# Optimization experiments

Measured on AMD Instinct MI355X. Metric: run time of the kernel, lower is better.

Reference implementation:

```python
import jax, jax.numpy as jnp
import numpy as np

D_IN, D_MODEL = 512, 256
B, N = 2, 512


def setup_inputs() -> dict:
    key = jax.random.key(0)
    ks = jax.random.split(key, 8)
    xav_x = float(np.sqrt(2.0 / (D_IN + D_MODEL)))
    xav_p = float(np.sqrt(2.0 / (4 + D_MODEL)))
    return {
        "x": jax.random.normal(ks[0], (B, N, D_IN), dtype=jnp.float32),
        "pos": jax.random.normal(ks[1], (B, N, 4), dtype=jnp.float32),
        "attn_mask": jax.random.randint(ks[2], (B, N, N), 0, 2, dtype=jnp.int32),
        "Wx": jax.random.normal(ks[3], (D_IN, D_MODEL), dtype=jnp.float32) * xav_x,
        "bx": jnp.zeros((D_MODEL,), dtype=jnp.float32),
        "Wp": jax.random.normal(ks[4], (4, D_MODEL), dtype=jnp.float32) * xav_p,
        "bp": jnp.zeros((D_MODEL,), dtype=jnp.float32),
        "w": jax.random.normal(ks[5], (D_MODEL,), dtype=jnp.float32) * 0.05,
    }


def reference(x, pos, attn_mask, Wx, bx, Wp, bp, w):
    # projected, activated inputs: [B, N, d_model]
    h = jnp.tanh(x @ Wx + bx)
    # pairwise relative positions: [B, N, N, 4]
    rel = pos[:, :, None, :] - pos[:, None, :, :]
    # position MLP + tanh: [B, N, N, d_model]
    z = jnp.tanh(rel @ Wp + bp)
    # scores via dot with weight vector: [B, N, N]
    attn = jnp.einsum("bijd,d->bij", z, w)
    mask = attn_mask != 0
    attn = jnp.where(mask, attn, -jnp.inf)
    attn = jax.nn.softmax(attn, axis=2)
    attn = jnp.where(mask, attn, 0.0)
    # dropout is identity in eval mode
    # weighted sum: [B, N, d_model]
    output = jnp.einsum("bij,bjd->bid", attn, h)
    return (output, attn)
```

## Files before the change

### kernel.cpp

```cpp
#include <hip/hip_runtime.h>
#include <hip/hip_bf16.h>
#include <math.h>

#define BATCH   2
#define SEQ     512
#define DIN     512
#define DM      256

#define LOG2E2  2.88539008177792681f

#if __has_builtin(__builtin_amdgcn_exp2f)
#define EXP2(x) __builtin_amdgcn_exp2f(x)
#else
#define EXP2(x) exp2f(x)
#endif
#if __has_builtin(__builtin_amdgcn_rcpf)
#define RCP(x) __builtin_amdgcn_rcpf(x)
#else
#define RCP(x) (1.0f / (x))
#endif

__device__ __forceinline__ float tanh_from_scaled(float targ) {
    return fmaf(-2.0f, RCP(1.0f + EXP2(targ)), 1.0f);
}

__global__ __launch_bounds__(512) void produce_k(
    const float* __restrict__ pos,
    const float* __restrict__ Wp,
    const float* __restrict__ x,
    const float* __restrict__ Wx,
    const float* __restrict__ bx,
    float* __restrict__ EBf,
    float* __restrict__ h)
{
    const int tid = threadIdx.x;

    if (blockIdx.x < 128) {
        const int b  = blockIdx.x >> 6;
        const int q  = blockIdx.x & 63;
        const int d0 = 4 * q;
        const float4 p = ((const float4*)pos)[b * SEQ + tid];
        #pragma unroll
        for (int i = 0; i < 4; i++) {
            const int d = d0 + i;
            const float P = fmaf(p.x, Wp[d], fmaf(p.y, Wp[DM + d],
                            fmaf(p.z, Wp[2*DM + d], p.w * Wp[3*DM + d])));
            EBf[((size_t)(b * DM + d)) * SEQ + tid] = EXP2(-LOG2E2 * P);
        }
        return;
    }

    __shared__ float  s_xt[2][32][68];
    __shared__ float  s_wt[2][64][32];
    __shared__ float4 s_part[256];

    const int idx = blockIdx.x - 128;
    const int rt  = idx >> 3;
    const int ct  = idx & 7;
    const int kh  = __builtin_amdgcn_readfirstlane(tid >> 8);
    const int t   = tid & 255;
    const int ty  = t >> 3;
    const int tx  = t & 7;
    const int row = rt * 32 + ty;

    float4 acc = make_float4(0.f, 0.f, 0.f, 0.f);

    for (int ks = 0; ks < 4; ks++) {
        const int k0 = kh * 256 + ks * 64;
        #pragma unroll
        for (int s = 0; s < 2; s++) {
            const int fidx = t * 2 + s;
            const int r = fidx >> 4, c = fidx & 15;
            *(float4*)&s_xt[kh][r][4 * c] =
                *(const float4*)(x + (size_t)(rt * 32 + r) * DIN + k0 + 4 * c);
        }
        #pragma unroll
        for (int s = 0; s < 2; s++) {
            const int fidx = t * 2 + s;
            const int r = fidx >> 3, c = fidx & 7;
            *(float4*)&s_wt[kh][r][4 * c] =
                *(const float4*)(Wx + (size_t)(k0 + r) * DM + ct * 32 + 4 * c);
        }
        __syncthreads();

        #pragma unroll 8
        for (int k = 0; k < 64; k++) {
            const float  xv = s_xt[kh][ty][k];
            const float4 wq = *(const float4*)&s_wt[kh][k][4 * tx];
            acc.x = fmaf(xv, wq.x, acc.x);
            acc.y = fmaf(xv, wq.y, acc.y);
            acc.z = fmaf(xv, wq.z, acc.z);
            acc.w = fmaf(xv, wq.w, acc.w);
        }
        __syncthreads();
    }

    if (kh == 1) s_part[t] = acc;
    __syncthreads();
    if (kh == 0) {
        const float4 q4 = s_part[t];
        const float4 bq = *(const float4*)(bx + ct * 32 + 4 * tx);
        float4 o;
        o.x = tanh_from_scaled(LOG2E2 * (acc.x + q4.x + bq.x));
        o.y = tanh_from_scaled(LOG2E2 * (acc.y + q4.y + bq.y));
        o.z = tanh_from_scaled(LOG2E2 * (acc.z + q4.z + bq.z));
        o.w = tanh_from_scaled(LOG2E2 * (acc.w + q4.w + bq.w));
        *(float4*)(h + (size_t)row * DM + ct * 32 + 4 * tx) = o;
    }
}

__global__ __launch_bounds__(512) void attend_k(
    const float* __restrict__ pos,
    const float* __restrict__ Wp,
    const float* __restrict__ bp,
    const int*   __restrict__ mask,
    const float* __restrict__ wv,
    const float* __restrict__ EBf,
    const float* __restrict__ h,
    float* __restrict__ out,
    float* __restrict__ attn_out)
{
    const int b   = blockIdx.x >> 7;
    const int i0  = (blockIdx.x & 127) * 4;
    const int tid = threadIdx.x;
    const int l   = tid & 63;

    __shared__ float4 s_ea[DM];
    __shared__ float  s_p[4][SEQ];
    __shared__ float  s_red[4][8];
    __shared__ float  s_o[7][4][DM];

    {
        const int d  = tid & 255;
        const int rp = __builtin_amdgcn_readfirstlane(tid >> 8);
        const int r0 = rp * 2;
        const float4 p0 = ((const float4*)pos)[b * SEQ + i0 + r0];
        const float4 p1 = ((const float4*)pos)[b * SEQ + i0 + r0 + 1];
        const float wp0 = Wp[d], wp1 = Wp[DM + d], wp2 = Wp[2*DM + d], wp3 = Wp[3*DM + d];
        const float bpd = bp[d];
        const float P0 = fmaf(p0.x, wp0, fmaf(p0.y, wp1, fmaf(p0.z, wp2, p0.w * wp3)));
        const float P1 = fmaf(p1.x, wp0, fmaf(p1.y, wp1, fmaf(p1.z, wp2, p1.w * wp3)));
        float* se = (float*)&s_ea[d];
        se[r0]     = EXP2(LOG2E2 * (P0 + bpd));
        se[r0 + 1] = EXP2(LOG2E2 * (P1 + bpd));
    }
    __syncthreads();

    const float* __restrict__ EBj = EBf + (size_t)b * DM * SEQ + tid;

    float a0 = 0.f, a1 = 0.f, a2 = 0.f, a3 = 0.f;
    #pragma unroll 8
    for (int t = 0; t < 128; t++) {
        const float eb0 = EBj[(size_t)(2*t) * SEQ];
        const float eb1 = EBj[(size_t)(2*t + 1) * SEQ];
        const float4 eA = s_ea[2*t];
        const float4 eB = s_ea[2*t + 1];
        const float w0 = wv[2*t];
        const float w1 = wv[2*t + 1];

        {
            const float y0 = fmaf(eA.x, eb0, 1.f), y1 = fmaf(eB.x, eb1, 1.f);
            a0 = fmaf(fmaf(w0, y1, w1 * y0), RCP(y0 * y1), a0);
        }
        {
            const float y0 = fmaf(eA.y, eb0, 1.f), y1 = fmaf(eB.y, eb1, 1.f);
            a1 = fmaf(fmaf(w0, y1, w1 * y0), RCP(y0 * y1), a1);
        }
        {
            const float y0 = fmaf(eA.z, eb0, 1.f), y1 = fmaf(eB.z, eb1, 1.f);
            a2 = fmaf(fmaf(w0, y1, w1 * y0), RCP(y0 * y1), a2);
        }
        {
            const float y0 = fmaf(eA.w, eb0, 1.f), y1 = fmaf(eB.w, eb1, 1.f);
            a3 = fmaf(fmaf(w0, y1, w1 * y0), RCP(y0 * y1), a3);
        }
    }

    const size_t mrow = (size_t)b * SEQ * SEQ + (size_t)i0 * SEQ + tid;
    const int m0 = mask[mrow];
    const int m1 = mask[mrow + SEQ];
    const int m2 = mask[mrow + 2*SEQ];
    const int m3 = mask[mrow + 3*SEQ];
    float p0 = m0 ? EXP2(-LOG2E2 * a0) : 0.f;
    float p1 = m1 ? EXP2(-LOG2E2 * a1) : 0.f;
    float p2 = m2 ? EXP2(-LOG2E2 * a2) : 0.f;
    float p3 = m3 ? EXP2(-LOG2E2 * a3) : 0.f;

    float s0 = p0, s1 = p1, s2 = p2, s3 = p3;
    #pragma unroll
    for (int off = 32; off; off >>= 1) {
        s0 += __shfl_xor(s0, off, 64);
        s1 += __shfl_xor(s1, off, 64);
        s2 += __shfl_xor(s2, off, 64);
        s3 += __shfl_xor(s3, off, 64);
    }
    const int w = tid >> 6;
    if (l == 0) { s_red[0][w] = s0; s_red[1][w] = s1; s_red[2][w] = s2; s_red[3][w] = s3; }
    __syncthreads();

    {
        const float4 r0a = ((const float4*)s_red[0])[0], r0b = ((const float4*)s_red[0])[1];
        const float4 r1a = ((const float4*)s_red[1])[0], r1b = ((const float4*)s_red[1])[1];
        const float4 r2a = ((const float4*)s_red[2])[0], r2b = ((const float4*)s_red[2])[1];
        const float4 r3a = ((const float4*)s_red[3])[0], r3b = ((const float4*)s_red[3])[1];
        p0 *= __fdividef(1.0f, (r0a.x+r0a.y+r0a.z+r0a.w) + (r0b.x+r0b.y+r0b.z+r0b.w));
        p1 *= __fdividef(1.0f, (r1a.x+r1a.y+r1a.z+r1a.w) + (r1b.x+r1b.y+r1b.z+r1b.w));
        p2 *= __fdividef(1.0f, (r2a.x+r2a.y+r2a.z+r2a.w) + (r2b.x+r2b.y+r2b.z+r2b.w));
        p3 *= __fdividef(1.0f, (r3a.x+r3a.y+r3a.z+r3a.w) + (r3b.x+r3b.y+r3b.z+r3b.w));
    }

    attn_out[mrow]         = p0;
    attn_out[mrow + SEQ]   = p1;
    attn_out[mrow + 2*SEQ] = p2;
    attn_out[mrow + 3*SEQ] = p3;
    s_p[0][tid] = p0; s_p[1][tid] = p1; s_p[2][tid] = p2; s_p[3][tid] = p3;
    __syncthreads();

    const int dq = tid & 63;
    const int js = __builtin_amdgcn_readfirstlane(tid >> 6);
    const float* __restrict__ hp = h + (size_t)(b * SEQ + js * 64) * DM + 4 * dq;
    const float* __restrict__ q0p = &s_p[0][js * 64];
    const float* __restrict__ q1p = &s_p[1][js * 64];
    const float* __restrict__ q2p = &s_p[2][js * 64];
    const float* __restrict__ q3p = &s_p[3][js * 64];

    float4 a0v = make_float4(0,0,0,0), a1v = a0v, a2v = a0v, a3v = a0v;
    #pragma unroll 4
    for (int jj = 0; jj < 16; jj++) {
        const float4 P0 = *(const float4*)(q0p + 4 * jj);
        const float4 P1 = *(const float4*)(q1p + 4 * jj);
        const float4 P2 = *(const float4*)(q2p + 4 * jj);
        const float4 P3 = *(const float4*)(q3p + 4 * jj);
        const float4 h0 = *(const float4*)(hp + (size_t)(4*jj + 0) * DM);
        const float4 h1 = *(const float4*)(hp + (size_t)(4*jj + 1) * DM);
        const float4 h2 = *(const float4*)(hp + (size_t)(4*jj + 2) * DM);
        const float4 h3 = *(const float4*)(hp + (size_t)(4*jj + 3) * DM);

        a0v.x = fmaf(P0.x,h0.x,fmaf(P0.y,h1.x,fmaf(P0.z,h2.x,fmaf(P0.w,h3.x,a0v.x))));
        a0v.y = fmaf(P0.x,h0.y,fmaf(P0.y,h1.y,fmaf(P0.z,h2.y,fmaf(P0.w,h3.y,a0v.y))));
        a0v.z = fmaf(P0.x,h0.z,fmaf(P0.y,h1.z,fmaf(P0.z,h2.z,fmaf(P0.w,h3.z,a0v.z))));
        a0v.w = fmaf(P0.x,h0.w,fmaf(P0.y,h1.w,fmaf(P0.z,h2.w,fmaf(P0.w,h3.w,a0v.w))));
        a1v.x = fmaf(P1.x,h0.x,fmaf(P1.y,h1.x,fmaf(P1.z,h2.x,fmaf(P1.w,h3.x,a1v.x))));
        a1v.y = fmaf(P1.x,h0.y,fmaf(P1.y,h1.y,fmaf(P1.z,h2.y,fmaf(P1.w,h3.y,a1v.y))));
        a1v.z = fmaf(P1.x,h0.z,fmaf(P1.y,h1.z,fmaf(P1.z,h2.z,fmaf(P1.w,h3.z,a1v.z))));
        a1v.w = fmaf(P1.x,h0.w,fmaf(P1.y,h1.w,fmaf(P1.z,h2.w,fmaf(P1.w,h3.w,a1v.w))));
        a2v.x = fmaf(P2.x,h0.x,fmaf(P2.y,h1.x,fmaf(P2.z,h2.x,fmaf(P2.w,h3.x,a2v.x))));
        a2v.y = fmaf(P2.x,h0.y,fmaf(P2.y,h1.y,fmaf(P2.z,h2.y,fmaf(P2.w,h3.y,a2v.y))));
        a2v.z = fmaf(P2.x,h0.z,fmaf(P2.y,h1.z,fmaf(P2.z,h2.z,fmaf(P2.w,h3.z,a2v.z))));
        a2v.w = fmaf(P2.x,h0.w,fmaf(P2.y,h1.w,fmaf(P2.z,h2.w,fmaf(P2.w,h3.w,a2v.w))));
        a3v.x = fmaf(P3.x,h0.x,fmaf(P3.y,h1.x,fmaf(P3.z,h2.x,fmaf(P3.w,h3.x,a3v.x))));
        a3v.y = fmaf(P3.x,h0.y,fmaf(P3.y,h1.y,fmaf(P3.z,h2.y,fmaf(P3.w,h3.y,a3v.y))));
        a3v.z = fmaf(P3.x,h0.z,fmaf(P3.y,h1.z,fmaf(P3.z,h2.z,fmaf(P3.w,h3.z,a3v.z))));
        a3v.w = fmaf(P3.x,h0.w,fmaf(P3.y,h1.w,fmaf(P3.z,h2.w,fmaf(P3.w,h3.w,a3v.w))));
    }

    if (js > 0) {
        *(float4*)&s_o[js - 1][0][4 * dq] = a0v;
        *(float4*)&s_o[js - 1][1][4 * dq] = a1v;
        *(float4*)&s_o[js - 1][2][4 * dq] = a2v;
        *(float4*)&s_o[js - 1][3][4 * dq] = a3v;
    }
    __syncthreads();
    if (js == 0) {
        #pragma unroll
        for (int s = 0; s < 7; s++) {
            const float4 q0 = *(const float4*)&s_o[s][0][4 * dq];
            const float4 q1 = *(const float4*)&s_o[s][1][4 * dq];
            const float4 q2 = *(const float4*)&s_o[s][2][4 * dq];
            const float4 q3 = *(const float4*)&s_o[s][3][4 * dq];
            a0v.x += q0.x; a0v.y += q0.y; a0v.z += q0.z; a0v.w += q0.w;
            a1v.x += q1.x; a1v.y += q1.y; a1v.z += q1.z; a1v.w += q1.w;
            a2v.x += q2.x; a2v.y += q2.y; a2v.z += q2.z; a2v.w += q2.w;
            a3v.x += q3.x; a3v.y += q3.y; a3v.z += q3.z; a3v.w += q3.w;
        }
        float* __restrict__ op = out + (size_t)(b * SEQ + i0) * DM + 4 * dq;
        *(float4*)(op)        = a0v;
        *(float4*)(op + DM)   = a1v;
        *(float4*)(op + 2*DM) = a2v;
        *(float4*)(op + 3*DM) = a3v;
    }
}

extern "C" void kernel_launch(void* const* d_in, const int* in_sizes, int n_in,
                              void* d_out, int out_size, void* d_ws, size_t ws_size,
                              hipStream_t stream) {
    const float* x    = (const float*)d_in[0];
    const float* pos  = (const float*)d_in[1];
    const int*   mask = (const int*)  d_in[2];
    const float* Wx   = (const float*)d_in[3];
    const float* bx   = (const float*)d_in[4];
    const float* Wp   = (const float*)d_in[5];
    const float* bp   = (const float*)d_in[6];
    const float* wv   = (const float*)d_in[7];

    float* out      = (float*)d_out;
    float* attn_out = (float*)d_out + (size_t)BATCH*SEQ*DM;

    char*  ws  = (char*)d_ws;
    float* h   = (float*)(ws);
    float* EBf = (float*)(ws + (size_t)BATCH*SEQ*DM*4);

    produce_k<<<384, 512, 0, stream>>>(pos, Wp, x, Wx, bx, EBf, h);
    attend_k <<<(BATCH*SEQ)/4, 512, 0, stream>>>(pos, Wp, bp, mask, wv, EBf, h, out, attn_out);
}
```

Before: 106.8 us.

## Fuse produce and attend kernels into one cooperative launch with grid sync

Merges the two kernels into a single cooperative kernel of 256 blocks. Each block first does the EBf/GEMM producer work (the first 128 blocks also compute EBf), then synchronizes the whole grid and reuses one shared buffer for the attention phase. The goal is to remove the second launch and the gap between kernels, at the cost of a grid-wide barrier and cooperative-launch constraints on residency.

```diff
diff --git a/kernel.cpp b/kernel.cpp
--- a/kernel.cpp
+++ b/kernel.cpp
@@ -1,6 +1,9 @@
 #include <hip/hip_runtime.h>
 #include <hip/hip_bf16.h>
+#include <hip/hip_cooperative_groups.h>
 #include <math.h>
+
+namespace cg = cooperative_groups;
 
 #define BATCH   2
 #define SEQ     512
@@ -24,15 +27,24 @@
     return fmaf(-2.0f, RCP(1.0f + EXP2(targ)), 1.0f);
 }
 
-__global__ __launch_bounds__(512) void produce_k(
+#define SMEM_BYTES 54272
+
+__global__ __launch_bounds__(512) void fused_k(
     const float* __restrict__ pos,
     const float* __restrict__ Wp,
+    const float* __restrict__ bp,
+    const int*   __restrict__ mask,
+    const float* __restrict__ wv,
     const float* __restrict__ x,
     const float* __restrict__ Wx,
     const float* __restrict__ bx,
     float* __restrict__ EBf,
-    float* __restrict__ h)
+    float* __restrict__ h,
+    float* __restrict__ out,
+    float* __restrict__ attn_out)
 {
+    __shared__ __align__(16) char smem[SMEM_BYTES];
+
     const int tid = threadIdx.x;
 
     if (blockIdx.x < 128) {
@@ -47,88 +59,78 @@
                             fmaf(p.z, Wp[2*DM + d], p.w * Wp[3*DM + d])));
             EBf[((size_t)(b * DM + d)) * SEQ + tid] = EXP2(-LOG2E2 * P);
         }
-        return;
-    }
-
-    __shared__ float  s_xt[2][32][68];
-    __shared__ float  s_wt[2][64][32];
-    __shared__ float4 s_part[256];
-
-    const int idx = blockIdx.x - 128;
-    const int rt  = idx >> 3;
-    const int ct  = idx & 7;
-    const int kh  = __builtin_amdgcn_readfirstlane(tid >> 8);
-    const int t   = tid & 255;
-    const int ty  = t >> 3;
-    const int tx  = t & 7;
-    const int row = rt * 32 + ty;
-
-    float4 acc = make_float4(0.f, 0.f, 0.f, 0.f);
-
-    for (int ks = 0; ks < 4; ks++) {
-        const int k0 = kh * 256 + ks * 64;
-        #pragma unroll
-        for (int s = 0; s < 2; s++) {
-            const int fidx = t * 2 + s;
-            const int r = fidx >> 4, c = fidx & 15;
-            *(float4*)&s_xt[kh][r][4 * c] =
-                *(const float4*)(x + (size_t)(rt * 32 + r) * DIN + k0 + 4 * c);
-        }
-        #pragma unroll
-        for (int s = 0; s < 2; s++) {
-            const int fidx = t * 2 + s;
-            const int r = fidx >> 3, c = fidx & 7;
-            *(float4*)&s_wt[kh][r][4 * c] =
-                *(const float4*)(Wx + (size_t)(k0 + r) * DM + ct * 32 + 4 * c);
-        }
+    }
+
+    {
+        float (*s_xt)[32][68] = (float(*)[32][68])(smem);
+        float (*s_wt)[64][32] = (float(*)[64][32])(smem + 17408);
+        float4* s_part        = (float4*)(smem + 17408 + 32768);
+
+        const int idx = blockIdx.x;
+        const int rt  = idx >> 3;
+        const int ct  = idx & 7;
+        const int kh  = __builtin_amdgcn_readfirstlane(tid >> 8);
+        const int t   = tid & 255;
+        const int ty  = t >> 3;
+        const int tx  = t & 7;
+        const int row = rt * 32 + ty;
+
+        float4 acc = make_float4(0.f, 0.f, 0.f, 0.f);
+
+        for (int ks = 0; ks < 4; ks++) {
+            const int k0 = kh * 256 + ks * 64;
+            #pragma unroll
+            for (int s = 0; s < 2; s++) {
+                const int fidx = t * 2 + s;
+                const int r = fidx >> 4, c = fidx & 15;
+                *(float4*)&s_xt[kh][r][4 * c] =
+                    *(const float4*)(x + (size_t)(rt * 32 + r) * DIN + k0 + 4 * c);
+            }
+            #pragma unroll
+            for (int s = 0; s < 2; s++) {
+                const int fidx = t * 2 + s;
+                const int r = fidx >> 3, c = fidx & 7;
+                *(float4*)&s_wt[kh][r][4 * c] =
+                    *(const float4*)(Wx + (size_t)(k0 + r) * DM + ct * 32 + 4 * c);
+            }
+            __syncthreads();
+
+            #pragma unroll 8
+            for (int k = 0; k < 64; k++) {
+                const float  xv = s_xt[kh][ty][k];
+                const float4 wq = *(const float4*)&s_wt[kh][k][4 * tx];
+                acc.x = fmaf(xv, wq.x, acc.x);
+                acc.y = fmaf(xv, wq.y, acc.y);
+                acc.z = fmaf(xv, wq.z, acc.z);
+                acc.w = fmaf(xv, wq.w, acc.w);
+            }
+            __syncthreads();
+        }
+
+        if (kh == 1) s_part[t] = acc;
         __syncthreads();
-
-        #pragma unroll 8
-        for (int k = 0; k < 64; k++) {
-            const float  xv = s_xt[kh][ty][k];
-            const float4 wq = *(const float4*)&s_wt[kh][k][4 * tx];
-            acc.x = fmaf(xv, wq.x, acc.x);
-            acc.y = fmaf(xv, wq.y, acc.y);
-            acc.z = fmaf(xv, wq.z, acc.z);
-            acc.w = fmaf(xv, wq.w, acc.w);
-        }
-        __syncthreads();
-    }
-
-    if (kh == 1) s_part[t] = acc;
-    __syncthreads();
-    if (kh == 0) {
-        const float4 q4 = s_part[t];
-        const float4 bq = *(const float4*)(bx + ct * 32 + 4 * tx);
-        float4 o;
-        o.x = tanh_from_scaled(LOG2E2 * (acc.x + q4.x + bq.x));
-        o.y = tanh_from_scaled(LOG2E2 * (acc.y + q4.y + bq.y));
-        o.z = tanh_from_scaled(LOG2E2 * (acc.z + q4.z + bq.z));
-        o.w = tanh_from_scaled(LOG2E2 * (acc.w + q4.w + bq.w));
-        *(float4*)(h + (size_t)row * DM + ct * 32 + 4 * tx) = o;
-    }
-}
-
-__global__ __launch_bounds__(512) void attend_k(
-    const float* __restrict__ pos,
-    const float* __restrict__ Wp,
-    const float* __restrict__ bp,
-    const int*   __restrict__ mask,
-    const float* __restrict__ wv,
-    const float* __restrict__ EBf,
-    const float* __restrict__ h,
-    float* __restrict__ out,
-    float* __restrict__ attn_out)
-{
-    const int b   = blockIdx.x >> 7;
-    const int i0  = (blockIdx.x & 127) * 4;
-    const int tid = threadIdx.x;
-    const int l   = tid & 63;
-
-    __shared__ float4 s_ea[DM];
-    __shared__ float  s_p[4][SEQ];
-    __shared__ float  s_red[4][8];
-    __shared__ float  s_o[7][4][DM];
+        if (kh == 0) {
+            const float4 q4 = s_part[t];
+            const float4 bq = *(const float4*)(bx + ct * 32 + 4 * tx);
+            float4 o;
+            o.x = tanh_from_scaled(LOG2E2 * (acc.x + q4.x + bq.x));
+            o.y = tanh_from_scaled(LOG2E2 * (acc.y + q4.y + bq.y));
+            o.z = tanh_from_scaled(LOG2E2 * (acc.z + q4.z + bq.z));
+            o.w = tanh_from_scaled(LOG2E2 * (acc.w + q4.w + bq.w));
+            *(float4*)(h + (size_t)row * DM + ct * 32 + 4 * tx) = o;
+        }
+    }
+
+    cg::this_grid().sync();
+
+    float4* s_ea        = (float4*)(smem);
+    float (*s_p)[SEQ]   = (float(*)[SEQ])(smem + 4096);
+    float (*s_red)[8]   = (float(*)[8])(smem + 12288);
+    float (*s_o)[4][DM] = (float(*)[4][DM])(smem + 12416);
+
+    const int b  = blockIdx.x >> 7;
+    const int i0 = (blockIdx.x & 127) * 4;
+    const int l  = tid & 63;
 
     {
         const int d  = tid & 255;
@@ -300,6 +302,11 @@
     float* h   = (float*)(ws);
     float* EBf = (float*)(ws + (size_t)BATCH*SEQ*DM*4);
 
-    produce_k<<<384, 512, 0, stream>>>(pos, Wp, x, Wx, bx, EBf, h);
-    attend_k <<<(BATCH*SEQ)/4, 512, 0, stream>>>(pos, Wp, bp, mask, wv, EBf, h, out, attn_out);
+    void* kargs[] = {
+        (void*)&pos, (void*)&Wp, (void*)&bp, (void*)&mask, (void*)&wv,
+        (void*)&x, (void*)&Wx, (void*)&bx, (void*)&EBf, (void*)&h,
+        (void*)&out, (void*)&attn_out
+    };
+    hipLaunchCooperativeKernel((const void*)fused_k, dim3(256), dim3(512),
+                               kargs, 0, stream);
 }
```

New measurement: 153.7 us. +44.0%, slower.
